# Performance work log

Hardware: AMD Instinct MI355X
Metric: run time of the kernel (lower is better)

The kernel has to match this reference:

```python
import jax, jax.numpy as jnp
import numpy as np

DN = ('NCHW', 'OIHW', 'NCHW')
SCALES = (4, 2, 5, 2, 1914)  # per-feature one-hot widths; sum=1927, +1 scalar row = 1928 CNN channels


def conv(x, w, b, stride):
    y = jax.lax.conv_general_dilated(x, w, stride, 'VALID', dimension_numbers=DN)
    return y + b[None, :, None, None]


def maxpool(x, window):
    return jax.lax.reduce_window(x, -jnp.inf, jax.lax.max, (1, 1) + window, (1, 1) + window, 'VALID')


def setup_inputs() -> dict:
    key = jax.random.key(0)
    ks = jax.random.split(key, 16)
    B, T, F, H, W = 2, 32, 8, 128, 128
    replay = jax.random.randint(ks[0], (B, T, F, H, W), 0, 2).astype(jnp.float32)

    def rn(k, shape, scale=0.02):
        return jax.random.normal(k, shape, jnp.float32) * scale

    return dict(
        replay_tensor=replay,
        emb_table=rn(ks[1], (16384, 200), 1.0),
        conv_con_w=rn(ks[2], (1, 1, 4, 4)), conv_con_b=jnp.zeros((1,), jnp.float32),
        fc_con_w=rn(ks[3], (200, 961)), fc_con_b=jnp.zeros((200,), jnp.float32),
        cnn1_w=rn(ks[4], (964, 1928, 1, 2)), cnn1_b=jnp.zeros((964,), jnp.float32),
        cnn2_w=rn(ks[5], (482, 964, 1, 2)), cnn2_b=jnp.zeros((482,), jnp.float32),
        cnn3_w=rn(ks[6], (241, 482, 1, 2)), cnn3_b=jnp.zeros((241,), jnp.float32),
        cnn4_w=rn(ks[7], (100, 241, 1, 2)), cnn4_b=jnp.zeros((100,), jnp.float32),
        fc_cnn_w=rn(ks[8], (100, 2300)), fc_cnn_b=jnp.zeros((100,), jnp.float32),
        lstm_w_ih=rn(ks[9], (400, 100), 0.1), lstm_w_hh=rn(ks[10], (400, 100), 0.1),
        lstm_b_ih=jnp.zeros((400,), jnp.float32), lstm_b_hh=jnp.zeros((400,), jnp.float32),
        fc_out_w=rn(ks[11], (2, 100), 0.1), fc_out_b=jnp.zeros((2,), jnp.float32),
        batch_size=2,
    )


def reference(replay_tensor, emb_table, conv_con_w, conv_con_b, fc_con_w, fc_con_b,
              cnn1_w, cnn1_b, cnn2_w, cnn2_b, cnn3_w, cnn3_b, cnn4_w, cnn4_b,
              fc_cnn_w, fc_cnn_b, lstm_w_ih, lstm_w_hh, lstm_b_ih, lstm_b_hh,
              fc_out_w, fc_out_b, batch_size):
    # np.delete(replay, 2, 2) then np.delete(., 3, 2) removes original features 2 and 4
    replay = replay_tensor[:batch_size, :, jnp.array([0, 1, 3, 5, 6, 7])]
    B, T = replay.shape[0], replay.shape[1]
    scalar = replay[:, :, 0]   # [B,T,128,128]
    cat = replay[:, :, 1:6]    # [B,T,5,128,128]

    # --- categorical branch ---
    # The original builds a [scale_k, H*W] one-hot scatter per (b,t,k), then the
    # embedding step reads only spatial column 0: row s of the per-feature block is
    # emb_table[1] iff value_at_pos0 == s (nonzero after thresholding), else emb_table[0].
    v0 = cat[:, :, :, 0, 0].astype(jnp.int32)  # [B,T,5]
    embs = []
    for k, sc in enumerate(SCALES):
        v = v0[:, :, k]
        v = jnp.where(v > sc, 0, v)  # threshold: values > scale_ zeroed
        idx = ((jnp.arange(sc)[None, None, :] == v[:, :, None]) & (v[:, :, None] != 0)).astype(jnp.int32)
        embs.append(emb_table[idx])  # [B,T,sc,200]
    emb_full = jnp.concatenate(embs, axis=2)  # [B,T,1927,200]

    # --- scalar conv branch (faithful to the bug: cnn_con2 applied to raw x) ---
    x = scalar.reshape(B * T, 1, 128, 128)
    y = maxpool(jax.nn.relu(conv(x, conv_con_w, conv_con_b, (2, 2))), (2, 2))  # [BT,1,31,31]
    y = y.reshape(B * T, -1) @ fc_con_w.T + fc_con_b                           # [BT,200]
    sca_full = y.reshape(B, T, 1, 200)

    # --- CNN over concatenated [1928, 1, 200] frames ---
    z = jnp.concatenate([sca_full, emb_full], axis=2).reshape(B * T, 1928, 1, 200)
    z = maxpool(jax.nn.relu(conv(z, cnn1_w, cnn1_b, (1, 1))), (1, 2))
    z = maxpool(jax.nn.relu(conv(z, cnn2_w, cnn2_b, (1, 1))), (1, 2))
    z = maxpool(jax.nn.relu(conv(z, cnn3_w, cnn3_b, (1, 1))), (1, 2))
    z = jax.nn.relu(conv(z, cnn4_w, cnn4_b, (1, 1)))  # [BT,100,1,23]
    z = z.reshape(B * T, -1) @ fc_cnn_w.T + fc_cnn_b  # [BT,100]
    seq = z.reshape(B, T, 100)

    # --- single-layer LSTM (torch gate order i,f,g,o), zero init state ---
    def step(carry, x_t):
        h, c = carry
        g = x_t @ lstm_w_ih.T + h @ lstm_w_hh.T + lstm_b_ih + lstm_b_hh
        i, f, gg, o = jnp.split(g, 4, axis=-1)
        c = jax.nn.sigmoid(f) * c + jax.nn.sigmoid(i) * jnp.tanh(gg)
        h = jax.nn.sigmoid(o) * jnp.tanh(c)
        return (h, c), None

    h0 = jnp.zeros((B, 100), seq.dtype)
    c0 = jnp.zeros((B, 100), seq.dtype)
    (hT, _), _ = jax.lax.scan(step, (h0, c0), jnp.swapaxes(seq, 0, 1))
    return hT @ fc_out_w.T + fc_out_b  # [B,2]
```

## Files before the change

### kernel.cpp

```cpp
#include <hip/hip_runtime.h>
#include <math.h>

#define DEVFN __device__ __forceinline__

typedef __bf16 bf16x8 __attribute__((ext_vector_type(8)));
typedef float f32x4 __attribute__((ext_vector_type(4)));

constexpr int T_ = 32;
constexpr int HW = 128;
constexpr int C1IN = 1928;
constexpr int C1 = 964;

DEVFN float sigm(float x) { return 1.0f / (1.0f + __expf(-x)); }
DEVFN float tanhfast(float x) { return 2.0f / (1.0f + __expf(-2.0f * x)) - 1.0f; }

DEVFN ushort f2b(float v) {
    union { float f; unsigned u; } x; x.f = v;
    unsigned r = x.u + 0x7fffu + ((x.u >> 16) & 1u);
    return (ushort)(r >> 16);
}

DEVFN void gload16(const ushort* g, ushort* l) {
    __builtin_amdgcn_global_load_lds(
        (const __attribute__((address_space(1))) unsigned int*)g,
        (__attribute__((address_space(3))) unsigned int*)l, 16, 0, 0);
}

__global__ void k_sca_conv(const float* __restrict__ replay, const float* __restrict__ wc,
                           const float* __restrict__ bc, float* __restrict__ y) {
    const int n = blockIdx.x;
    const int idx = blockIdx.y * 256 + threadIdx.x;
    if (idx >= 961) return;
    const float* x = replay + (size_t)n * 8 * HW * HW;
    float wr_[16];
    #pragma unroll
    for (int t = 0; t < 16; ++t) wr_[t] = wc[t];
    const float bcv = bc[0];
    const int i = idx / 31, j = idx % 31;
    float m = 0.0f;
    #pragma unroll
    for (int di = 0; di < 2; ++di)
    #pragma unroll
    for (int dj = 0; dj < 2; ++dj) {
        const int h0 = 2 * (2 * i + di), w0 = 2 * (2 * j + dj);
        float acc = bcv;
        #pragma unroll
        for (int p = 0; p < 4; ++p)
        #pragma unroll
        for (int q = 0; q < 4; ++q)
            acc += x[(h0 + p) * HW + (w0 + q)] * wr_[p * 4 + q];
        m = fmaxf(m, fmaxf(acc, 0.0f));
    }
    y[n * 961 + idx] = m;
}

__global__ void k_sca_fc(const float* __restrict__ y, const float* __restrict__ fcw,
                         const float* __restrict__ fcb, float* __restrict__ sca) {
    const int n = blockIdx.x;
    const int wid = threadIdx.x >> 6, lane = threadIdx.x & 63;
    const int o = blockIdx.y * 4 + wid;
    float acc = 0.f;
    for (int m = lane; m < 961; m += 64)
        acc += y[n * 961 + m] * fcw[(size_t)o * 961 + m];
    #pragma unroll
    for (int off = 32; off > 0; off >>= 1) acc += __shfl_down(acc, off);
    if (lane == 0) sca[n * 200 + o] = acc + fcb[o];
}

__global__ void k_prep(const float* __restrict__ w1, const float* __restrict__ w2,
                       const float* __restrict__ w3, const float* __restrict__ w4,
                       const float* __restrict__ whh, const float* __restrict__ replay,
                       float* __restrict__ wsum, float* __restrict__ sa,
                       ushort* __restrict__ A2, ushort* __restrict__ A3,
                       ushort* __restrict__ A4, float* __restrict__ whhT) {
    const int bid = blockIdx.x;
    const int tx = threadIdx.x;
    constexpr int N2 = 2 * 512 * 1024;
    constexpr int N3 = 2 * 256 * 512;
    constexpr int N4 = 2 * 128 * 256;
    if (bid < 5533) {
        const int idx = bid * 256 + tx;
        if (idx < N2) {
            const int kw = idx >> 19;
            const int r = idx & 524287;
            const int oc = r >> 10, ic = r & 1023;
            const float v = (oc < 482 && ic < 964) ? w2[(size_t)oc * 1928 + ic * 2 + kw] : 0.f;
            A2[idx] = f2b(v);
        } else if (idx < N2 + N3) {
            const int j = idx - N2;
            const int kw = j >> 17;
            const int r = j & 131071;
            const int oc = r >> 9, ic = r & 511;
            const float v = (oc < 241 && ic < 482) ? w3[(size_t)oc * 964 + ic * 2 + kw] : 0.f;
            A3[j] = f2b(v);
        } else if (idx < N2 + N3 + N4) {
            const int j = idx - (N2 + N3);
            const int kw = j >> 15;
            const int r = j & 32767;
            const int oc = r >> 8, ic = r & 255;
            const float v = (oc < 100 && ic < 241) ? w4[(size_t)oc * 482 + ic * 2 + kw] : 0.f;
            A4[j] = f2b(v);
        } else {
            const int j = idx - (N2 + N3 + N4);
            if (j < 40000) {
                const int m = j / 400, p = j - m * 400;
                const int go = (p & 3) * 100 + (p >> 2);
                whhT[m * 400 + p] = whh[go * 100 + m];
            }
        }
    } else if (bid < 5774) {
        const int oc = (bid - 5533) * 4 + (tx >> 6);
        const int lane = tx & 63;
        const float* wr = w1 + (size_t)oc * C1IN * 2;
        float s0 = 0.f, s1 = 0.f;
        for (int ic = lane; ic < C1IN; ic += 64) {
            s0 += wr[ic * 2 + 0];
            s1 += wr[ic * 2 + 1];
        }
        #pragma unroll
        for (int off = 32; off > 0; off >>= 1) {
            s0 += __shfl_down(s0, off);
            s1 += __shfl_down(s1, off);
        }
        if (lane == 0) { wsum[oc * 2] = s0; wsum[oc * 2 + 1] = s1; }
    } else {
        const int j = bid - 5774;
        const int n = j >> 2;
        const int oc = (j & 3) * 256 + tx;
        if (oc < C1) {
            const int chs[5]    = {1, 3, 5, 6, 7};
            const int scales[5] = {4, 2, 5, 2, 1914};
            const int offs[5]   = {0, 4, 6, 11, 13};
            float s0 = 0.f, s1 = 0.f;
            #pragma unroll
            for (int k = 0; k < 5; ++k) {
                int v = (int)replay[((size_t)n * 8 + chs[k]) * HW * HW];
                if (v > scales[k]) v = 0;
                if (v >= 1 && v <= scales[k] - 1) {
                    const int ic = 1 + offs[k] + v;
                    s0 += w1[((size_t)oc * C1IN + ic) * 2 + 0];
                    s1 += w1[((size_t)oc * C1IN + ic) * 2 + 1];
                }
            }
            sa[(n * C1 + oc) * 2 + 0] = s0;
            sa[(n * C1 + oc) * 2 + 1] = s1;
        }
    }
}

template <int OCT>
__global__ void k_cnn1(const float* __restrict__ sca, const float* __restrict__ emb,
                       const float* __restrict__ w1, const float* __restrict__ b1,
                       const float* __restrict__ wsum, const float* __restrict__ sa,
                       ushort* __restrict__ Bt2) {
    const int n = blockIdx.x;
    const int ocBase = blockIdx.y * OCT;
    const int tx = threadIdx.x;
    __shared__ float ev[200], sv[200], dv[200];
    __shared__ float oscal[OCT][7];
    __shared__ float vals[OCT][100];
    for (int i = tx; i < 200; i += blockDim.x) {
        const float e0 = emb[i], e1 = emb[200 + i];
        ev[i] = e0;
        dv[i] = e1 - e0;
        sv[i] = sca[n * 200 + i] - e0;
    }
    for (int i = tx; i < OCT * 7; i += blockDim.x) {
        const int ocl = i / 7, f = i % 7;
        const int oc = ocBase + ocl;
        float v = 0.f;
        if (oc < C1) {
            switch (f) {
                case 0: v = wsum[oc * 2 + 0]; break;
                case 1: v = wsum[oc * 2 + 1]; break;
                case 2: v = b1[oc]; break;
                case 3: v = w1[(size_t)oc * C1IN * 2 + 0]; break;
                case 4: v = w1[(size_t)oc * C1IN * 2 + 1]; break;
                case 5: v = sa[(n * C1 + oc) * 2 + 0]; break;
                case 6: v = sa[(n * C1 + oc) * 2 + 1]; break;
            }
        }
        oscal[ocl][f] = v;
    }
    __syncthreads();
    for (int item = tx; item < OCT * 99; item += blockDim.x) {
        const int ocl = item / 99, u = item % 99;
        const int oc = ocBase + ocl;
        float res = 0.f;
        if (oc < C1) {
            const float ws0 = oscal[ocl][0], ws1 = oscal[ocl][1], bb = oscal[ocl][2];
            const float a0 = oscal[ocl][3], a1 = oscal[ocl][4];
            const float s0 = oscal[ocl][5], s1 = oscal[ocl][6];
            float r = -INFINITY;
            #pragma unroll
            for (int dw = 0; dw < 2; ++dw) {
                const int ww = 2 * u + dw;
                const float o = bb + ws0 * ev[ww] + ws1 * ev[ww + 1]
                                   + a0 * sv[ww] + a1 * sv[ww + 1]
                                   + s0 * dv[ww] + s1 * dv[ww + 1];
                r = fmaxf(r, o);
            }
            res = fmaxf(r, 0.0f);
        }
        vals[ocl][u] = res;
    }
    __syncthreads();
    for (int i = tx; i < OCT * 100; i += blockDim.x) {
        const int u = i >> 4, ocl = i & 15;
        const float v = (u < 99) ? vals[ocl][u] : 0.0f;
        Bt2[(size_t)(n * 100 + u) * 1024 + ocBase + ocl] = f2b(v);
    }
    if (n == 0 && ocBase == 0) {
        for (int i = tx; i < 1024; i += blockDim.x)
            Bt2[(size_t)6400 * 1024 + i] = 0;
    }
}

template <int OCREAL, int WR, int WOUT, int KICP, int MPAD, int OMODE, int OSTR,
          bool POOL, int MT, int NTILES>
__global__ __launch_bounds__(256, 2) void k_gemm_conv(
    const ushort* __restrict__ A, const ushort* __restrict__ Bt,
    const float* __restrict__ bias, void* __restrict__ outv) {
    constexpr int BK = 64;
    constexpr int NT = KICP / BK;
    constexpr int NWG = MT * NTILES;
    constexpr int Qq = NWG / 8, Rr = NWG % 8;

    __shared__ __align__(16) ushort As0[2][4096];
    __shared__ __align__(16) ushort As1[2][4096];
    __shared__ __align__(16) ushort Bs[2][8704];

    const int bid = blockIdx.x;
    const int xcd = bid & 7, rest = bid >> 3;
    const int base = (xcd < Rr) ? xcd * (Qq + 1) : Rr * (Qq + 1) + (xcd - Rr) * Qq;
    const int sid = base + rest;
    const int mBase = (sid % MT) * 64;
    const int nBase = (sid / MT) * 128;

    const int tx = threadIdx.x;
    const int wave = tx >> 6, lane = tx & 63;
    const int lr = lane & 15, lk = lane >> 4;
    const int r8 = lane >> 3;
    const int cx = (lane & 7) ^ r8;
    const ushort* A1p = A + (size_t)MPAD * KICP;

    f32x4 acc[4][2] = {};

    auto STAGE = [&](int buf, int kt) {
        const int k0 = kt * BK + cx * 8;
        #pragma unroll
        for (int it = 0; it < 2; ++it) {
            const int s = wave + it * 4;
            const int row = s * 8 + r8;
            gload16(&A[(size_t)(mBase + row) * KICP + k0], &As0[buf][s * 512]);
            gload16(&A1p[(size_t)(mBase + row) * KICP + k0], &As1[buf][s * 512]);
        }
        #pragma unroll
        for (int it = 0; it < 4; ++it) {
            const int s = wave + it * 4;
            const int row = s * 8 + r8;
            gload16(&Bt[(size_t)(nBase + row) * KICP + k0], &Bs[buf][s * 512]);
        }
        if (wave == 0) {
            const int row = 128 + r8;
            gload16(&Bt[(size_t)(nBase + row) * KICP + k0], &Bs[buf][16 * 512]);
        }
    };

    auto COMPUTE = [&](int cur) {
        #pragma unroll
        for (int ks = 0; ks < 2; ++ks) {
            bf16x8 a0[4], a1[4], b0[2], b1[2];
            #pragma unroll
            for (int i = 0; i < 4; ++i) {
                const int row = i * 16 + lr;
                const int col = (ks * 32 + lk * 8) ^ ((row & 7) << 3);
                a0[i] = *(const bf16x8*)&As0[cur][row * 64 + col];
                a1[i] = *(const bf16x8*)&As1[cur][row * 64 + col];
            }
            #pragma unroll
            for (int j = 0; j < 2; ++j) {
                const int row = wave * 32 + j * 16 + lr;
                const int col = (ks * 32 + lk * 8) ^ ((row & 7) << 3);
                b0[j] = *(const bf16x8*)&Bs[cur][row * 64 + col];
                const int row1 = row + 1;
                const int col1 = (ks * 32 + lk * 8) ^ ((row1 & 7) << 3);
                b1[j] = *(const bf16x8*)&Bs[cur][row1 * 64 + col1];
            }
            #pragma unroll
            for (int i = 0; i < 4; ++i)
                #pragma unroll
                for (int j = 0; j < 2; ++j) {
                    acc[i][j] = __builtin_amdgcn_mfma_f32_16x16x32_bf16(a0[i], b0[j], acc[i][j], 0, 0, 0);
                    acc[i][j] = __builtin_amdgcn_mfma_f32_16x16x32_bf16(a1[i], b1[j], acc[i][j], 0, 0, 0);
                }
        }
    };

    STAGE(0, 0);
    __syncthreads();
    #pragma unroll 1
    for (int kt = 0; kt < NT; ++kt) {
        const int cur = kt & 1;
        if (kt + 1 < NT) STAGE(cur ^ 1, kt + 1);
        COMPUTE(cur);
        __syncthreads();
    }

    ushort* outb = (ushort*)outv;
    float*  outf = (float*)outv;
    constexpr int NOUTW = POOL ? (WOUT / 2) : WOUT;
    constexpr int WRN = NOUTW + 1;
    constexpr int NVALID = WR * 64;
    #pragma unroll
    for (int i = 0; i < 4; ++i) {
        const int m0 = mBase + i * 16 + lk * 4;
        #pragma unroll
        for (int j = 0; j < 2; ++j) {
            const int r = nBase + wave * 32 + j * 16 + lr;
            const int n = r / WR, w = r - n * WR;
            #pragma unroll
            for (int reg = 0; reg < 4; ++reg) {
                const float v = acc[i][j][reg];
                const float vo = __shfl_xor(v, 1);
                const int m = m0 + reg;
                const bool lok = POOL ? ((lr & 1) == 0) : true;
                if (lok && (w < WOUT) && (m < OCREAL) && (r < NVALID)) {
                    const float pre = POOL ? fmaxf(v, vo) : v;
                    const float val = fmaxf(pre + bias[m], 0.0f);
                    const int wc = POOL ? (w >> 1) : w;
                    if (OMODE == 2)
                        outb[((size_t)(n * WRN + wc)) * OSTR + m] = f2b(val);
                    else
                        outf[((size_t)n * OCREAL + m) * NOUTW + wc] = val;
                }
            }
        }
    }
}

__global__ void k_fc_cnn(const float* __restrict__ z4, const float* __restrict__ w,
                         const float* __restrict__ b, float* __restrict__ seq) {
    const int n = blockIdx.x;
    const int wid = threadIdx.x >> 6, lane = threadIdx.x & 63;
    const int o = blockIdx.y * 4 + wid;
    const float4* zr = (const float4*)(z4 + (size_t)n * 2300);
    const float4* wr = (const float4*)(w + (size_t)o * 2300);
    float acc = 0.f;
    for (int m = lane; m < 575; m += 64) {
        const float4 wv = wr[m];
        const float4 zv = zr[m];
        acc += wv.x * zv.x + wv.y * zv.y + wv.z * zv.z + wv.w * zv.w;
    }
    #pragma unroll
    for (int off = 32; off > 0; off >>= 1) acc += __shfl_down(acc, off);
    if (lane == 0) seq[n * 100 + o] = acc + b[o];
}

__global__ void k_xg(const float* __restrict__ seq, const float* __restrict__ wih,
                     const float* __restrict__ bih, const float* __restrict__ bhh,
                     float* __restrict__ xg) {
    const int n = blockIdx.x;
    __shared__ __align__(16) float s[100];
    if (threadIdx.x < 100) s[threadIdx.x] = seq[n * 100 + threadIdx.x];
    __syncthreads();
    const int p = threadIdx.x;
    if (p < 400) {
        const int go = (p & 3) * 100 + (p >> 2);
        const float4* wr = (const float4*)(wih + (size_t)go * 100);
        const float4* s4 = (const float4*)s;
        float4 a = {0.f, 0.f, 0.f, 0.f};
        #pragma unroll
        for (int m = 0; m < 25; ++m) {
            const float4 wv = wr[m];
            const float4 sv = s4[m];
            a.x += wv.x * sv.x; a.y += wv.y * sv.y;
            a.z += wv.z * sv.z; a.w += wv.w * sv.w;
        }
        xg[n * 400 + p] = bih[go] + bhh[go] + a.x + a.y + a.z + a.w;
    }
}

__global__ __launch_bounds__(448) void k_lstm(const float* __restrict__ xg,
                                              const float* __restrict__ whhT,
                                              const float* __restrict__ fw,
                                              const float* __restrict__ fb,
                                              float* __restrict__ outp) {
    const int bb = blockIdx.x;
    const int tx = threadIdx.x;
    __shared__ __align__(16) float hb[2][104];
    float wreg[100];
    if (tx < 400) {
        #pragma unroll
        for (int m = 0; m < 100; ++m) wreg[m] = whhT[m * 400 + tx];
    }
    float creg = 0.f;
    if (tx < 104) { hb[0][tx] = 0.f; hb[1][tx] = 0.f; }
    float xnext = (tx < 400) ? xg[(size_t)(bb * T_) * 400 + tx] : 0.f;
    __syncthreads();
    const int lane = tx & 63, base = lane & ~3;
    const int g = tx & 3;
    for (int t = 0; t < T_; ++t) {
        float act = 0.f;
        if (tx < 400) {
            float a0 = xnext, a1 = 0.f, a2 = 0.f, a3 = 0.f;
            if (t + 1 < T_) xnext = xg[(size_t)(bb * T_ + t + 1) * 400 + tx];
            const float4* h4 = (const float4*)&hb[t & 1][0];
            #pragma unroll
            for (int m4 = 0; m4 < 25; ++m4) {
                const float4 hv = h4[m4];
                a0 += hv.x * wreg[4 * m4 + 0];
                a1 += hv.y * wreg[4 * m4 + 1];
                a2 += hv.z * wreg[4 * m4 + 2];
                a3 += hv.w * wreg[4 * m4 + 3];
            }
            const float accv = (a0 + a1) + (a2 + a3);
            act = (g == 2) ? tanhfast(accv) : sigm(accv);
        }
        const float aI = __shfl(act, base + 0);
        const float aF = __shfl(act, base + 1);
        const float aG = __shfl(act, base + 2);
        const float aO = __shfl(act, base + 3);
        if (tx < 400) {
            const float cn = aF * creg + aI * aG;
            creg = cn;
            if (g == 0) hb[(t + 1) & 1][tx >> 2] = aO * tanhfast(cn);
        }
        __syncthreads();
    }
    if (tx < 2) {
        float acc = fb[tx];
        for (int j = 0; j < 100; ++j) acc += hb[0][j] * fw[tx * 100 + j];
        outp[bb * 2 + tx] = acc;
    }
}

extern "C" void kernel_launch(void* const* d_in, const int* in_sizes, int n_in,
                              void* d_out, int out_size, void* d_ws, size_t ws_size,
                              hipStream_t stream) {
    (void)in_sizes; (void)n_in; (void)out_size; (void)ws_size;
    const float* replay = (const float*)d_in[0];
    const float* emb    = (const float*)d_in[1];
    const float* ccw    = (const float*)d_in[2];
    const float* ccb    = (const float*)d_in[3];
    const float* fcw    = (const float*)d_in[4];
    const float* fcb    = (const float*)d_in[5];
    const float* w1     = (const float*)d_in[6];
    const float* b1     = (const float*)d_in[7];
    const float* w2     = (const float*)d_in[8];
    const float* b2     = (const float*)d_in[9];
    const float* w3     = (const float*)d_in[10];
    const float* b3     = (const float*)d_in[11];
    const float* w4     = (const float*)d_in[12];
    const float* b4     = (const float*)d_in[13];
    const float* fcnw   = (const float*)d_in[14];
    const float* fcnb   = (const float*)d_in[15];
    const float* wih    = (const float*)d_in[16];
    const float* whh    = (const float*)d_in[17];
    const float* bih    = (const float*)d_in[18];
    const float* bhh    = (const float*)d_in[19];
    const float* fow    = (const float*)d_in[20];
    const float* fob    = (const float*)d_in[21];

    float* ws = (float*)d_ws;
    float*  sca  = ws + 0;
    float*  wsum = ws + 12800;
    float*  sa   = ws + 14848;
    float*  seq  = ws + 138240;
    float*  xg   = ws + 144640;
    float*  whhT = ws + 170240;
    float*  yb   = ws + 210240;
    float*  z4   = ws + 272384;
    ushort* A2   = (ushort*)(ws + 419584);
    ushort* A3   = (ushort*)(ws + 943872);
    ushort* A4   = (ushort*)(ws + 1074944);
    ushort* Bt2  = (ushort*)(ws + 1107712);
    ushort* Bt3  = (ushort*)(ws + 4385024);
    ushort* Bt4  = (ushort*)(ws + 5208320);
    float*  outp = (float*)d_out;

    k_sca_conv<<<dim3(64, 4), 256, 0, stream>>>(replay, ccw, ccb, yb);
    k_sca_fc<<<dim3(64, 50), 256, 0, stream>>>(yb, fcw, fcb, sca);
    k_prep<<<6030, 256, 0, stream>>>(w1, w2, w3, w4, whh, replay,
                                     wsum, sa, A2, A3, A4, whhT);
    k_cnn1<16><<<dim3(64, 64), 256, 0, stream>>>(sca, emb, w1, b1, wsum, sa, Bt2);
    k_gemm_conv<482, 100, 98, 1024, 512, 2, 512, true, 8, 50>
        <<<400, 256, 0, stream>>>(A2, Bt2, b2, Bt3);
    k_gemm_conv<241, 50, 48, 512, 256, 2, 256, true, 4, 25>
        <<<100, 256, 0, stream>>>(A3, Bt3, b3, Bt4);
    k_gemm_conv<100, 25, 23, 256, 128, 0, 0, false, 2, 13>
        <<<26, 256, 0, stream>>>(A4, Bt4, b4, z4);
    k_fc_cnn<<<dim3(64, 25), 256, 0, stream>>>(z4, fcnw, fcnb, seq);
    k_xg<<<64, 512, 0, stream>>>(seq, wih, bih, bhh, xg);
    k_lstm<<<2, 448, 0, stream>>>(xg, whhT, fow, fob, outp);
}
```

Measured before the change: 142.2 us.

## Fuse scalar conv/fc into prep kernel, fold xg into LSTM, deepen GEMM prefetch

```diff
diff --git a/kernel.cpp b/kernel.cpp
--- a/kernel.cpp
+++ b/kernel.cpp
@@ -26,60 +26,59 @@
         (__attribute__((address_space(3))) unsigned int*)l, 16, 0, 0);
 }
 
-__global__ void k_sca_conv(const float* __restrict__ replay, const float* __restrict__ wc,
-                           const float* __restrict__ bc, float* __restrict__ y) {
-    const int n = blockIdx.x;
-    const int idx = blockIdx.y * 256 + threadIdx.x;
-    if (idx >= 961) return;
-    const float* x = replay + (size_t)n * 8 * HW * HW;
-    float wr_[16];
-    #pragma unroll
-    for (int t = 0; t < 16; ++t) wr_[t] = wc[t];
-    const float bcv = bc[0];
-    const int i = idx / 31, j = idx % 31;
-    float m = 0.0f;
-    #pragma unroll
-    for (int di = 0; di < 2; ++di)
-    #pragma unroll
-    for (int dj = 0; dj < 2; ++dj) {
-        const int h0 = 2 * (2 * i + di), w0 = 2 * (2 * j + dj);
-        float acc = bcv;
-        #pragma unroll
-        for (int p = 0; p < 4; ++p)
-        #pragma unroll
-        for (int q = 0; q < 4; ++q)
-            acc += x[(h0 + p) * HW + (w0 + q)] * wr_[p * 4 + q];
-        m = fmaxf(m, fmaxf(acc, 0.0f));
-    }
-    y[n * 961 + idx] = m;
-}
-
-__global__ void k_sca_fc(const float* __restrict__ y, const float* __restrict__ fcw,
-                         const float* __restrict__ fcb, float* __restrict__ sca) {
-    const int n = blockIdx.x;
-    const int wid = threadIdx.x >> 6, lane = threadIdx.x & 63;
-    const int o = blockIdx.y * 4 + wid;
-    float acc = 0.f;
-    for (int m = lane; m < 961; m += 64)
-        acc += y[n * 961 + m] * fcw[(size_t)o * 961 + m];
-    #pragma unroll
-    for (int off = 32; off > 0; off >>= 1) acc += __shfl_down(acc, off);
-    if (lane == 0) sca[n * 200 + o] = acc + fcb[o];
-}
-
-__global__ void k_prep(const float* __restrict__ w1, const float* __restrict__ w2,
-                       const float* __restrict__ w3, const float* __restrict__ w4,
-                       const float* __restrict__ whh, const float* __restrict__ replay,
-                       float* __restrict__ wsum, float* __restrict__ sa,
-                       ushort* __restrict__ A2, ushort* __restrict__ A3,
-                       ushort* __restrict__ A4, float* __restrict__ whhT) {
+__global__ __launch_bounds__(512) void k_sca_prep(
+    const float* __restrict__ replay, const float* __restrict__ ccw,
+    const float* __restrict__ ccb, const float* __restrict__ fcw,
+    const float* __restrict__ fcb, const float* __restrict__ w1,
+    const float* __restrict__ w2, const float* __restrict__ w3,
+    const float* __restrict__ w4, const float* __restrict__ whh,
+    float* __restrict__ sca, float* __restrict__ wsum, float* __restrict__ sa,
+    ushort* __restrict__ A2, ushort* __restrict__ A3, ushort* __restrict__ A4,
+    float* __restrict__ whhT) {
     const int bid = blockIdx.x;
     const int tx = threadIdx.x;
     constexpr int N2 = 2 * 512 * 1024;
     constexpr int N3 = 2 * 256 * 512;
     constexpr int N4 = 2 * 128 * 256;
-    if (bid < 5533) {
-        const int idx = bid * 256 + tx;
+    __shared__ __align__(16) float ys[961];
+    __shared__ float wcs[16];
+
+    if (bid < 64) {
+        const int n = bid;
+        const float* x = replay + (size_t)n * 8 * HW * HW;
+        if (tx < 16) wcs[tx] = ccw[tx];
+        __syncthreads();
+        const float bcv = ccb[0];
+        for (int idx = tx; idx < 961; idx += 512) {
+            const int i = idx / 31, j = idx % 31;
+            float m = 0.0f;
+            #pragma unroll
+            for (int di = 0; di < 2; ++di)
+            #pragma unroll
+            for (int dj = 0; dj < 2; ++dj) {
+                const int h0 = 2 * (2 * i + di), w0 = 2 * (2 * j + dj);
+                float acc = bcv;
+                #pragma unroll
+                for (int p = 0; p < 4; ++p)
+                #pragma unroll
+                for (int q = 0; q < 4; ++q)
+                    acc += x[(h0 + p) * HW + (w0 + q)] * wcs[p * 4 + q];
+                m = fmaxf(m, fmaxf(acc, 0.0f));
+            }
+            ys[idx] = m;
+        }
+        __syncthreads();
+        const int wid = tx >> 6, lane = tx & 63;
+        for (int o = wid; o < 200; o += 8) {
+            float acc = 0.f;
+            const float* wr = fcw + (size_t)o * 961;
+            for (int m = lane; m < 961; m += 64) acc += ys[m] * wr[m];
+            #pragma unroll
+            for (int off = 32; off > 0; off >>= 1) acc += __shfl_down(acc, off);
+            if (lane == 0) sca[n * 200 + o] = acc + fcb[o];
+        }
+    } else if (bid < 2831) {
+        const int idx = (bid - 64) * 512 + tx;
         if (idx < N2) {
             const int kw = idx >> 19;
             const int r = idx & 524287;
@@ -108,25 +107,27 @@
                 whhT[m * 400 + p] = whh[go * 100 + m];
             }
         }
-    } else if (bid < 5774) {
-        const int oc = (bid - 5533) * 4 + (tx >> 6);
+    } else if (bid < 2952) {
+        const int oc = (bid - 2831) * 8 + (tx >> 6);
         const int lane = tx & 63;
-        const float* wr = w1 + (size_t)oc * C1IN * 2;
-        float s0 = 0.f, s1 = 0.f;
-        for (int ic = lane; ic < C1IN; ic += 64) {
-            s0 += wr[ic * 2 + 0];
-            s1 += wr[ic * 2 + 1];
-        }
-        #pragma unroll
-        for (int off = 32; off > 0; off >>= 1) {
-            s0 += __shfl_down(s0, off);
-            s1 += __shfl_down(s1, off);
-        }
-        if (lane == 0) { wsum[oc * 2] = s0; wsum[oc * 2 + 1] = s1; }
+        if (oc < C1) {
+            const float* wr = w1 + (size_t)oc * C1IN * 2;
+            float s0 = 0.f, s1 = 0.f;
+            for (int ic = lane; ic < C1IN; ic += 64) {
+                s0 += wr[ic * 2 + 0];
+                s1 += wr[ic * 2 + 1];
+            }
+            #pragma unroll
+            for (int off = 32; off > 0; off >>= 1) {
+                s0 += __shfl_down(s0, off);
+                s1 += __shfl_down(s1, off);
+            }
+            if (lane == 0) { wsum[oc * 2] = s0; wsum[oc * 2 + 1] = s1; }
+        }
     } else {
-        const int j = bid - 5774;
-        const int n = j >> 2;
-        const int oc = (j & 3) * 256 + tx;
+        const int j = bid - 2952;
+        const int n = j >> 1;
+        const int oc = (j & 1) * 512 + tx;
         if (oc < C1) {
             const int chs[5]    = {1, 3, 5, 6, 7};
             const int scales[5] = {4, 2, 5, 2, 1914};
@@ -298,13 +299,21 @@
     };
 
     STAGE(0, 0);
-    __syncthreads();
+    if (NT > 1) STAGE(1, 1);
     #pragma unroll 1
     for (int kt = 0; kt < NT; ++kt) {
         const int cur = kt & 1;
-        if (kt + 1 < NT) STAGE(cur ^ 1, kt + 1);
+        if (kt + 1 < NT) {
+            if (wave == 0) asm volatile("s_waitcnt vmcnt(9)" ::: "memory");
+            else           asm volatile("s_waitcnt vmcnt(8)" ::: "memory");
+        } else {
+            asm volatile("s_waitcnt vmcnt(0)" ::: "memory");
+        }
+        __builtin_amdgcn_sched_barrier(0);
+        __builtin_amdgcn_s_barrier();
         COMPUTE(cur);
-        __syncthreads();
+        __builtin_amdgcn_s_barrier();
+        if (kt + 2 < NT) STAGE(cur, kt + 2);
     }
 
     ushort* outb = (ushort*)outv;
@@ -357,54 +366,51 @@
     if (lane == 0) seq[n * 100 + o] = acc + b[o];
 }
 
-__global__ void k_xg(const float* __restrict__ seq, const float* __restrict__ wih,
-                     const float* __restrict__ bih, const float* __restrict__ bhh,
-                     float* __restrict__ xg) {
-    const int n = blockIdx.x;
-    __shared__ __align__(16) float s[100];
-    if (threadIdx.x < 100) s[threadIdx.x] = seq[n * 100 + threadIdx.x];
-    __syncthreads();
-    const int p = threadIdx.x;
-    if (p < 400) {
-        const int go = (p & 3) * 100 + (p >> 2);
-        const float4* wr = (const float4*)(wih + (size_t)go * 100);
-        const float4* s4 = (const float4*)s;
-        float4 a = {0.f, 0.f, 0.f, 0.f};
-        #pragma unroll
-        for (int m = 0; m < 25; ++m) {
-            const float4 wv = wr[m];
-            const float4 sv = s4[m];
-            a.x += wv.x * sv.x; a.y += wv.y * sv.y;
-            a.z += wv.z * sv.z; a.w += wv.w * sv.w;
-        }
-        xg[n * 400 + p] = bih[go] + bhh[go] + a.x + a.y + a.z + a.w;
-    }
-}
-
-__global__ __launch_bounds__(448) void k_lstm(const float* __restrict__ xg,
+__global__ __launch_bounds__(448) void k_lstm(const float* __restrict__ seq,
+                                              const float* __restrict__ wih,
+                                              const float* __restrict__ bih,
+                                              const float* __restrict__ bhh,
                                               const float* __restrict__ whhT,
                                               const float* __restrict__ fw,
                                               const float* __restrict__ fb,
                                               float* __restrict__ outp) {
     const int bb = blockIdx.x;
     const int tx = threadIdx.x;
+    __shared__ __align__(16) float sb[32][100];
+    __shared__ __align__(16) float xgs[32][400];
     __shared__ __align__(16) float hb[2][104];
     float wreg[100];
     if (tx < 400) {
         #pragma unroll
         for (int m = 0; m < 100; ++m) wreg[m] = whhT[m * 400 + tx];
     }
-    float creg = 0.f;
+    for (int i = tx; i < 3200; i += 448)
+        sb[i / 100][i % 100] = seq[(size_t)(bb * T_ + i / 100) * 100 + (i % 100)];
     if (tx < 104) { hb[0][tx] = 0.f; hb[1][tx] = 0.f; }
-    float xnext = (tx < 400) ? xg[(size_t)(bb * T_) * 400 + tx] : 0.f;
+    __syncthreads();
+    for (int idx = tx; idx < 12800; idx += 448) {
+        const int t = idx / 400, p = idx - t * 400;
+        const int go = (p & 3) * 100 + (p >> 2);
+        const float4* wr = (const float4*)(wih + (size_t)go * 100);
+        const float4* s4 = (const float4*)&sb[t][0];
+        float4 a = {0.f, 0.f, 0.f, 0.f};
+        #pragma unroll
+        for (int m = 0; m < 25; ++m) {
+            const float4 wv = wr[m];
+            const float4 sv = s4[m];
+            a.x += wv.x * sv.x; a.y += wv.y * sv.y;
+            a.z += wv.z * sv.z; a.w += wv.w * sv.w;
+        }
+        xgs[t][p] = bih[go] + bhh[go] + a.x + a.y + a.z + a.w;
+    }
     __syncthreads();
     const int lane = tx & 63, base = lane & ~3;
     const int g = tx & 3;
+    float creg = 0.f;
     for (int t = 0; t < T_; ++t) {
         float act = 0.f;
         if (tx < 400) {
-            float a0 = xnext, a1 = 0.f, a2 = 0.f, a3 = 0.f;
-            if (t + 1 < T_) xnext = xg[(size_t)(bb * T_ + t + 1) * 400 + tx];
+            float a0 = xgs[t][tx], a1 = 0.f, a2 = 0.f, a3 = 0.f;
             const float4* h4 = (const float4*)&hb[t & 1][0];
             #pragma unroll
             for (int m4 = 0; m4 < 25; ++m4) {
@@ -467,22 +473,19 @@
     float*  wsum = ws + 12800;
     float*  sa   = ws + 14848;
     float*  seq  = ws + 138240;
-    float*  xg   = ws + 144640;
-    float*  whhT = ws + 170240;
-    float*  yb   = ws + 210240;
-    float*  z4   = ws + 272384;
-    ushort* A2   = (ushort*)(ws + 419584);
-    ushort* A3   = (ushort*)(ws + 943872);
-    ushort* A4   = (ushort*)(ws + 1074944);
-    ushort* Bt2  = (ushort*)(ws + 1107712);
-    ushort* Bt3  = (ushort*)(ws + 4385024);
-    ushort* Bt4  = (ushort*)(ws + 5208320);
+    float*  whhT = ws + 144640;
+    float*  z4   = ws + 184640;
+    ushort* A2   = (ushort*)(ws + 331840);
+    ushort* A3   = (ushort*)(ws + 856128);
+    ushort* A4   = (ushort*)(ws + 987200);
+    ushort* Bt2  = (ushort*)(ws + 1019968);
+    ushort* Bt3  = (ushort*)(ws + 4297280);
+    ushort* Bt4  = (ushort*)(ws + 5120576);
     float*  outp = (float*)d_out;
 
-    k_sca_conv<<<dim3(64, 4), 256, 0, stream>>>(replay, ccw, ccb, yb);
-    k_sca_fc<<<dim3(64, 50), 256, 0, stream>>>(yb, fcw, fcb, sca);
-    k_prep<<<6030, 256, 0, stream>>>(w1, w2, w3, w4, whh, replay,
-                                     wsum, sa, A2, A3, A4, whhT);
+    k_sca_prep<<<3080, 512, 0, stream>>>(replay, ccw, ccb, fcw, fcb,
+                                         w1, w2, w3, w4, whh,
+                                         sca, wsum, sa, A2, A3, A4, whhT);
     k_cnn1<16><<<dim3(64, 64), 256, 0, stream>>>(sca, emb, w1, b1, wsum, sa, Bt2);
     k_gemm_conv<482, 100, 98, 1024, 512, 2, 512, true, 8, 50>
         <<<400, 256, 0, stream>>>(A2, Bt2, b2, Bt3);
@@ -491,6 +494,5 @@
     k_gemm_conv<100, 25, 23, 256, 128, 0, 0, false, 2, 13>
         <<<26, 256, 0, stream>>>(A4, Bt4, b4, z4);
     k_fc_cnn<<<dim3(64, 25), 256, 0, stream>>>(z4, fcnw, fcnb, seq);
-    k_xg<<<64, 512, 0, stream>>>(seq, wih, bih, bhh, xg);
-    k_lstm<<<2, 448, 0, stream>>>(xg, whhT, fow, fob, outp);
-}
+    k_lstm<<<2, 448, 0, stream>>>(seq, wih, bih, bhh, whhT, fow, fob, outp);
+}
```

Result: slower. 327.2 us (+130.1%).
